# Performance work log

Hardware: AMD Instinct MI355X
Metric: run time of the kernel (lower is better)

## Reference

```python
import jax, jax.numpy as jnp
import numpy as np

HEADS = 8

def conv1x1(x, w, b=None):
    # x: [b,c,h,w], w: [o,c]
    y = jnp.einsum('bchw,oc->bohw', x, w)
    if b is not None:
        y = y + b[None, :, None, None]
    return y

def dwconv3(x, w):
    # depthwise 3x3, SAME padding; w: [C,1,3,3]
    return jax.lax.conv_general_dilated(
        x, w, window_strides=(1, 1), padding='SAME',
        feature_group_count=x.shape[1],
        dimension_numbers=('NCHW', 'OIHW', 'NCHW'))

def layernorm_c(x, w, b):
    # WithBias LayerNorm over channel dim (torch normalizes last dim of b,(hw),c)
    mu = x.mean(axis=1, keepdims=True)
    var = ((x - mu) ** 2).mean(axis=1, keepdims=True)
    return (x - mu) / jnp.sqrt(var + 1e-5) * w[None, :, None, None] + b[None, :, None, None]

def l2norm_lastdim(x):
    n = jnp.sqrt(jnp.sum(x * x, axis=-1, keepdims=True))
    return x / jnp.maximum(n, 1e-12)

def channel_attention(xq, xkv, q_w, q_dw_w, kv_w, kv_dw_w, temperature, attn4, proj_w):
    b, c, h, w = xq.shape
    q = dwconv3(conv1x1(xq, q_w), q_dw_w)
    kv = dwconv3(conv1x1(xkv, kv_w), kv_dw_w)
    k, v = jnp.split(kv, 2, axis=1)
    ch = c // HEADS  # channels per head
    def heads(t):
        return t.reshape(b, HEADS, ch, h * w)
    q, k, v = heads(q), heads(k), heads(v)
    q = l2norm_lastdim(q)
    k = l2norm_lastdim(k)
    attn = jnp.einsum('bhcn,bhdn->bhcd', q, k) * temperature[None]  # [b,H,ch,ch]
    kk = int(ch * 0.9)
    thr = jax.lax.top_k(attn, kk)[0][..., -1:]
    masked = jnp.where(attn >= thr, attn, -jnp.inf)
    score = jax.nn.softmax(masked, axis=-1)
    out = jnp.einsum('bhcd,bhdn->bhcn', score, v) * attn4
    out = out.reshape(b, c, h, w)
    return conv1x1(out, proj_w)

def geglu_ffn(x, ffn_in_w, ffn_dw_w, ffn_out_w):
    y = conv1x1(x, ffn_in_w)
    y = dwconv3(y, ffn_dw_w)
    y1, y2 = jnp.split(y, 2, axis=1)
    return conv1x1(jax.nn.gelu(y1, approximate=False) * y2, ffn_out_w)


def reference(vi_featur, ir_featur, text_code,
              se_w1, se_w2, conv1x1_w, conv1x1_b, conv_out_w, conv_out_b,
              text_w1, text_b1, text_w2, text_b2,
              norm1_w, norm1_b, norm2_w, norm2_b, norm3_w, norm3_b,
              q_w, q_dw_w, kv_w, kv_dw_w, temperature, attn4, proj_w,
              ffn_in_w, ffn_dw_w, ffn_out_w):
    b, c, h, w = vi_featur.shape
    concat = jnp.concatenate([vi_featur, ir_featur], axis=1)  # [b,2c,h,w]
    squeeze = concat.mean(axis=(2, 3))                         # [b,2c]
    cw = jax.nn.sigmoid(jax.nn.relu(squeeze @ se_w1.T) @ se_w2.T)
    topk = c  # int(2*ch_dim*0.5)
    idx = jax.lax.top_k(cw, topk)[1]                           # [b,topk]
    selected = jnp.take_along_axis(concat, idx[:, :, None, None], axis=1)
    img = conv1x1(selected, conv1x1_w, conv1x1_b)              # [b,2c,h,w]
    tf = jax.nn.relu(text_code @ text_w1.T + text_b1) @ text_w2.T + text_b2  # [b,2c]
    soft_idx = jax.lax.top_k(tf, 2 * c)[1]                     # full descending perm
    shuffled = jnp.take_along_axis(img, soft_idx[:, :, None, None], axis=1)
    q_in = conv1x1(shuffled, conv_out_w, conv_out_b)           # [b,c,h,w]
    img_feature2 = conv1x1(concat, conv_out_w, conv_out_b)
    att = channel_attention(layernorm_c(q_in, norm1_w, norm1_b),
                            layernorm_c(img_feature2, norm2_w, norm2_b),
                            q_w, q_dw_w, kv_w, kv_dw_w, temperature, attn4, proj_w)
    output = att + geglu_ffn(layernorm_c(att, norm3_w, norm3_b), ffn_in_w, ffn_dw_w, ffn_out_w)
    return (output, img_feature2)


def setup_inputs() -> dict:
    key = jax.random.key(0)
    ks = jax.random.split(key, 20)
    B, C, H, W = 4, 128, 128, 128
    s = 0.05
    d = {
        'vi_featur': jax.random.normal(ks[0], (B, C, H, W), jnp.float32),
        'ir_featur': jax.random.normal(ks[1], (B, C, H, W), jnp.float32),
        'text_code': jax.random.normal(ks[2], (B, 512), jnp.float32),
        'se_w1': jax.random.normal(ks[3], (32, 256), jnp.float32) * s,
        'se_w2': jax.random.normal(ks[4], (256, 32), jnp.float32) * s,
        'conv1x1_w': jax.random.normal(ks[5], (256, 128), jnp.float32) * s,
        'conv1x1_b': jnp.zeros((256,), jnp.float32),
        'conv_out_w': jax.random.normal(ks[6], (128, 256), jnp.float32) * s,
        'conv_out_b': jnp.zeros((128,), jnp.float32),
        'text_w1': jax.random.normal(ks[7], (512, 512), jnp.float32) * s,
        'text_b1': jnp.zeros((512,), jnp.float32),
        'text_w2': jax.random.normal(ks[8], (256, 512), jnp.float32) * s,
        'text_b2': jnp.zeros((256,), jnp.float32),
        'norm1_w': jnp.ones((128,), jnp.float32), 'norm1_b': jnp.zeros((128,), jnp.float32),
        'norm2_w': jnp.ones((128,), jnp.float32), 'norm2_b': jnp.zeros((128,), jnp.float32),
        'norm3_w': jnp.ones((128,), jnp.float32), 'norm3_b': jnp.zeros((128,), jnp.float32),
        'q_w': jax.random.normal(ks[9], (128, 128), jnp.float32) * s,
        'q_dw_w': jax.random.normal(ks[10], (128, 1, 3, 3), jnp.float32) * s,
        'kv_w': jax.random.normal(ks[11], (256, 128), jnp.float32) * s,
        'kv_dw_w': jax.random.normal(ks[12], (256, 1, 3, 3), jnp.float32) * s,
        'temperature': jnp.ones((8, 1, 1), jnp.float32),
        'attn4': jnp.ones((1,), jnp.float32) * 0.2,
        'proj_w': jax.random.normal(ks[13], (128, 128), jnp.float32) * s,
        'ffn_in_w': jax.random.normal(ks[14], (680, 128), jnp.float32) * s,
        'ffn_dw_w': jax.random.normal(ks[15], (680, 1, 3, 3), jnp.float32) * s,
        'ffn_out_w': jax.random.normal(ks[16], (128, 340), jnp.float32) * s,
    }
    return d
```

## Files before the change

### kernel.cpp

```cpp
#include <hip/hip_runtime.h>

typedef unsigned short u16;
typedef __attribute__((ext_vector_type(8))) short bf16x8;
typedef __attribute__((ext_vector_type(4))) float f32x4;

#define N_PIX 16384
static constexpr long NP = 4L * 128 * N_PIX;

__device__ __forceinline__ float bf2f(u16 h) {
  unsigned u = ((unsigned)h) << 16; float f; __builtin_memcpy(&f, &u, 4); return f;
}
__device__ __forceinline__ u16 f2bf(float f) {
  unsigned u; __builtin_memcpy(&u, &f, 4);
  u = (u + 0x7fffu + ((u >> 16) & 1u)) >> 16; return (u16)u;
}

__device__ __forceinline__ float blockReduceSum256(float v) {
  #pragma unroll
  for (int o = 32; o > 0; o >>= 1) v += __shfl_down(v, o, 64);
  __shared__ float sw[4];
  int lane = threadIdx.x & 63, w = threadIdx.x >> 6;
  if (lane == 0) sw[w] = v;
  __syncthreads();
  return (threadIdx.x == 0) ? (sw[0] + sw[1] + sw[2] + sw[3]) : 0.f;
// ... 89 lines not shown
      #pragma unroll
      for (int o = 32; o > 0; o >>= 1) s += __shfl_down(s, o, 64);
      if (lane == 0) t1f[b * 512 + j] = fmaxf(s + tb1[j], 0.f);
    }
  }
}

__global__ __launch_bounds__(256) void text2_k(const float* __restrict__ t1f,
                                               const float* __restrict__ tw2,
                                               const float* __restrict__ tb2,
                                               float* __restrict__ tf) {
  int b = blockIdx.y, j0 = blockIdx.x * 8, tid = threadIdx.x;
  __shared__ float s_t1[512];
  s_t1[tid] = t1f[b * 512 + tid];
  s_t1[tid + 256] = t1f[b * 512 + 256 + tid];
  __syncthreads();
  int w = tid >> 6, lane = tid & 63;
  #pragma unroll
  for (int r = 0; r < 2; ++r) {
    int j = j0 + w * 2 + r;
    const float* wr = tw2 + (long)j * 512;
    float s = 0.f;
    #pragma unroll
    for (int k = 0; k < 8; ++k) s += s_t1[lane + k * 64] * wr[lane + k * 64];
    #pragma unroll
    for (int o = 32; o > 0; o >>= 1) s += __shfl_down(s, o, 64);
    if (lane == 0) tf[b * 256 + j] = s + tb2[j];
  }
}

__global__ __launch_bounds__(256) void rank2_k(const float* __restrict__ tf,
                                               int* __restrict__ sidx) {
  int b = blockIdx.x, tid = threadIdx.x;
  __shared__ float s_tf[256];
  s_tf[tid] = tf[b * 256 + tid];
  __syncthreads();
  float my = s_tf[tid];
  int rk = 0;
  for (int c = 0; c < 256; ++c) {
    float o = s_tf[c];
    rk += (o > my) || (o == my && c < tid);
  }
  sidx[b * 256 + rk] = tid;
}

__global__ __launch_bounds__(128) void mcomb_k(const float* __restrict__ w2,
                                               const float* __restrict__ w2b,
                                               const float* __restrict__ w1,
                                               const float* __restrict__ w1b,
                                               const int* __restrict__ idx,
                                               const int* __restrict__ sidx,
                                               u16* __restrict__ mch,
                                               u16* __restrict__ mcl,
                                               float* __restrict__ bcomb) {
  int o = blockIdx.x, b = blockIdx.y, tid = threadIdx.x;
  __shared__ float s_w2[256];
  __shared__ int s_sx[256];
  s_w2[tid] = w2[o * 256 + tid];
  s_w2[tid + 128] = w2[o * 256 + tid + 128];
  s_sx[tid] = sidx[b * 256 + tid] & 255;
  s_sx[tid + 128] = sidx[b * 256 + tid + 128] & 255;
  u16* hrow = mch + ((long)b * 128 + o) * 256;
  u16* lrow = mcl + ((long)b * 128 + o) * 256;
  hrow[tid] = 0; hrow[tid + 128] = 0;
  lrow[tid] = 0; lrow[tid + 128] = 0;
  __syncthreads();
  float s = 0.f;
  for (int j = 0; j < 256; ++j) s += s_w2[j] * w1[s_sx[j] * 128 + tid];
  int cc = idx[b * 128 + tid] & 255;
  u16 hi = f2bf(s);
  hrow[cc] = hi;
  lrow[cc] = f2bf(s - bf2f(hi));
  if (tid == 0) {
    float bb = w2b[o];
    for (int j = 0; j < 256; ++j) bb += s_w2[j] * w1b[s_sx[j]];
    bcomb[b * 128 + o] = bb;
  }
}

__global__ __launch_bounds__(256) void gemm_dual_k(
    const u16* __restrict__ W2b, const float* __restrict__ b2,
    const u16* __restrict__ Mch, const u16* __restrict__ Mcl,
    const float* __restrict__ bc, const u16* __restrict__ Xb,
    float* __restrict__ out1, u16* __restrict__ qinT, u16* __restrict__ img2T) {
  const int N = N_PIX;
  int n0 = blockIdx.x * 64, o0 = blockIdx.y * 64, bz = blockIdx.z, tid = threadIdx.x;
  __shared__ __align__(16) char smem[36864];
  u16* A1  = (u16*)smem;
  u16* A2h = (u16*)(smem + 9216);
  u16* A2l = (u16*)(smem + 18432);
  u16* Xs  = (u16*)(smem + 27648);
  f32x4 acc1[4], acc2[4];
  #pragma unroll
  for (int i = 0; i < 4; ++i) { acc1[i] = (f32x4){0,0,0,0}; acc2[i] = (f32x4){0,0,0,0}; }
  int wv = tid >> 6, lane = tid & 63;
  int lr = lane & 15, lkq = (lane >> 4) * 8;
  for (int kt = 0; kt < 4; ++kt) {
    int k0 = kt << 6;
    {
      int r = tid >> 2, o = o0 + r;
      #pragma unroll
      for (int cc = 0; cc < 2; ++cc) {
        int col = ((tid & 3) << 3) + cc * 32;
        int k = k0 + col;
        *(bf16x8*)&A1[r * 72 + col] = *(const bf16x8*)(W2b + (long)o * 256 + k);
        *(bf16x8*)&A2h[r * 72 + col] = *(const bf16x8*)(Mch + ((long)bz * 128 + o) * 256 + k);
        *(bf16x8*)&A2l[r * 72 + col] = *(const bf16x8*)(Mcl + ((long)bz * 128 + o) * 256 + k);
      }
    }
    {
      int n = tid & 63;
      const u16* src = Xb + (long)bz * 256 * N + n0 + n;
      #pragma unroll
      for (int cc = 0; cc < 2; ++cc) {
        int kb = ((tid >> 6) << 3) + cc * 32;
        int k = k0 + kb;
        bf16x8 t;
        #pragma unroll
        for (int i = 0; i < 8; ++i) t[i] = (short)src[(long)(k + i) * N];
        *(bf16x8*)&Xs[n * 72 + kb] = t;
      }
    }
    __syncthreads();
    #pragma unroll
    for (int kk = 0; kk < 2; ++kk) {
      int lk = kk * 32 + lkq;
      bf16x8 a1 = *(const bf16x8*)&A1[(wv * 16 + lr) * 72 + lk];
      bf16x8 a2h = *(const bf16x8*)&A2h[(wv * 16 + lr) * 72 + lk];
      bf16x8 a2l = *(const bf16x8*)&A2l[(wv * 16 + lr) * 72 + lk];
      #pragma unroll
      for (int nt = 0; nt < 4; ++nt) {
        bf16x8 bfr = *(const bf16x8*)&Xs[(nt * 16 + lr) * 72 + lk];
        acc1[nt] = __builtin_amdgcn_mfma_f32_16x16x32_bf16(a1, bfr, acc1[nt], 0, 0, 0);
        acc2[nt] = __builtin_amdgcn_mfma_f32_16x16x32_bf16(a2h, bfr, acc2[nt], 0, 0, 0);
        acc2[nt] = __builtin_amdgcn_mfma_f32_16x16x32_bf16(a2l, bfr, acc2[nt], 0, 0, 0);
      }
    }
    __syncthreads();
  }
  float* st1 = (float*)smem;
  u16*  stq = (u16*)(smem + 17408);
  u16*  sti = (u16*)(smem + 26112);
  #pragma unroll
  for (int nt = 0; nt < 4; ++nt)
    #pragma unroll
    for (int r4 = 0; r4 < 4; ++r4) {
      int o_l = wv * 16 + (lane >> 4) * 4 + r4;
      int n_l = nt * 16 + (lane & 15);
      float v1 = acc1[nt][r4] + b2[o0 + o_l];
      float v2 = acc2[nt][r4] + bc[bz * 128 + o0 + o_l];
      st1[o_l * 68 + n_l] = v1;
      stq[n_l * 68 + o_l] = f2bf(v2);
      sti[n_l * 68 + o_l] = f2bf(v1);
    }
  __syncthreads();
  {
    int row = tid >> 2, colb = (tid & 3) * 16;
    float* dst = out1 + ((long)bz * 128 + o0 + row) * N + n0 + colb;
    #pragma unroll
    for (int j = 0; j < 4; ++j)
      *(f32x4*)(dst + j * 4) = *(f32x4*)&st1[row * 68 + colb + j * 4];
    u16* dq = qinT + ((long)bz * N_PIX + n0 + row) * 128 + o0 + colb;
    u16* di = img2T + ((long)bz * N_PIX + n0 + row) * 128 + o0 + colb;
    *(bf16x8*)dq = *(bf16x8*)&stq[row * 68 + colb];
    *(bf16x8*)(dq + 8) = *(bf16x8*)&stq[row * 68 + colb + 8];
    *(bf16x8*)di = *(bf16x8*)&sti[row * 68 + colb];
    *(bf16x8*)(di + 8) = *(bf16x8*)&sti[row * 68 + colb + 8];
  }
}

__global__ __launch_bounds__(256) void lnrow_k(u16* __restrict__ t0, u16* __restrict__ t1,
                                               const float* __restrict__ g1, const float* __restrict__ b1,
                                               const float* __restrict__ g2, const float* __restrict__ b2) {
  int y = blockIdx.y, tid = threadIdx.x;
  u16* buf = y ? t1 : t0;
  const float* g = y ? g2 : g1;
  const float* bb = y ? b2 : b1;
  __shared__ float gs[128], bs[128];
  if (tid < 128) { gs[tid] = g[tid]; bs[tid] = bb[tid]; }
  __syncthreads();
  long p = (long)blockIdx.x * 256 + tid;
  u16* src = buf + p * 128;
  bf16x8 v[16];
  float sum = 0.f, sq = 0.f;
  #pragma unroll
  for (int j = 0; j < 16; ++j) {
    v[j] = *(const bf16x8*)(src + j * 8);
    #pragma unroll
    for (int i = 0; i < 8; ++i) { float f = bf2f((u16)v[j][i]); sum += f; sq += f * f; }
  }
  float mu = sum * (1.f / 128.f);
  float var = sq * (1.f / 128.f) - mu * mu;
  float rs = rsqrtf(fmaxf(var, 0.f) + 1e-5f);
  #pragma unroll
  for (int j = 0; j < 16; ++j) {
    bf16x8 r;
    #pragma unroll
    for (int i = 0; i < 8; ++i) {
      float f = bf2f((u16)v[j][i]);
      r[i] = (short)f2bf((f - mu) * rs * gs[j * 8 + i] + bs[j * 8 + i]);
    }
    *(bf16x8*)(src + j * 8) = r;
  }
}

template<int AMODE, int RESADD, int OUTF, int XT, int OT>
__global__ __launch_bounds__(256) void gemm_k(
    const u16* __restrict__ Ah, const u16* __restrict__ Alo, long a_bstride,
    const u16* __restrict__ X, long x_bstride,
    const u16* __restrict__ res, long res_bstride,
    void* __restrict__ outv, long out_bstride,
    int O, int K) {
  const int N = N_PIX;
  int n0 = blockIdx.x * 64;
  int o0 = blockIdx.y * 64 * OT;
  int bz = blockIdx.z;
  int tid = threadIdx.x;
  int wv = tid >> 6, lane = tid & 63;
  int lr = lane & 15, lkq = (lane >> 4) * 8;
  __shared__ __align__(16) u16 Xs[64][136];
  __shared__ __align__(16) u16 As[(XT == 3) ? 1 : 64][136];
  __shared__ __align__(16) u16 Al[(AMODE == 3) ? 64 : 1][136];
  f32x4 acc[OT][4];
  #pragma unroll
  for (int ot = 0; ot < OT; ++ot)
    #pragma unroll
    for (int i = 0; i < 4; ++i) acc[ot][i] = (f32x4){0.f, 0.f, 0.f, 0.f};

  if (XT == 3) {
    {
      int n = tid >> 2, koff = (tid & 3) << 5;
      const u16* src = X + (long)bz * x_bstride + (long)(n0 + n) * 128 + koff;
      #pragma unroll
      for (int j = 0; j < 4; ++j)
        *(bf16x8*)&Xs[n][koff + j * 8] = *(const bf16x8*)(src + j * 8);
    }
    __syncthreads();
    #pragma unroll
    for (int ot = 0; ot < OT; ++ot) {
      int oc = o0 + ot * 64 + wv * 16 + lr;
      if (oc > O - 1) oc = O - 1;
      const u16* Arow = Ah + (long)oc * 128;
      bf16x8 afr[4];
      #pragma unroll
      for (int kk = 0; kk < 4; ++kk) afr[kk] = *(const bf16x8*)(Arow + kk * 32 + lkq);
      #pragma unroll
      for (int kk = 0; kk < 4; ++kk) {
        int lk = kk * 32 + lkq;
        #pragma unroll
        for (int nt = 0; nt < 4; ++nt) {
          bf16x8 bfr = *(const bf16x8*)&Xs[nt * 16 + lr][lk];
          acc[ot][nt] = __builtin_amdgcn_mfma_f32_16x16x32_bf16(afr[kk], bfr, acc[ot][nt], 0, 0, 0);
        }
      }
    }
    __syncthreads();
  } else {
    int nk = (K + 127) >> 7;
    for (int kt = 0; kt < nk; ++kt) {
      int k0 = kt << 7;
      {
        int n = tid & 63;
        const u16* src = X + (long)bz * x_bstride + n0 + n;
        #pragma unroll
        for (int cc = 0; cc < 4; ++cc) {
          int kb = ((tid >> 6) << 3) + cc * 32;
          int k = k0 + kb;
          bf16x8 t;
          #pragma unroll
          for (int i = 0; i < 8; ++i)
            t[i] = (short)((k + i < K) ? src[(long)(k + i) * N] : (u16)0);
          *(bf16x8*)&Xs[n][kb] = t;
        }
      }
      #pragma unroll
      for (int ot = 0; ot < OT; ++ot) {
        {
          int r = tid >> 2, o = o0 + ot * 64 + r;
          #pragma unroll
          for (int cc = 0; cc < 4; ++cc) {
            int col = ((tid & 3) << 3) + cc * 32;
            int k = k0 + col;
            if (AMODE == 2) {
              bf16x8 t;
              if (o < O && k + 8 <= K) {
                t = *(const bf16x8*)(Ah + (long)o * K + k);
              } else {
                #pragma unroll
                for (int i = 0; i < 8; ++i)
                  t[i] = (short)((o < O && k + i < K) ? Ah[(long)o * K + k + i] : (u16)0);
              }
              *(bf16x8*)&As[r][col] = t;
            } else {
              long base = (long)bz * a_bstride + (long)o * K + k;
              *(bf16x8*)&As[r][col] = *(const bf16x8*)(Ah + base);
              *(bf16x8*)&Al[r][col] = *(const bf16x8*)(Alo + base);
            }
          }
        }
        __syncthreads();
        #pragma unroll
        for (int kk = 0; kk < 4; ++kk) {
          int lk = kk * 32 + lkq;
          bf16x8 afr = *(const bf16x8*)&As[wv * 16 + lr][lk];
          bf16x8 alr;
          if (AMODE == 3) alr = *(const bf16x8*)&Al[wv * 16 + lr][lk];
          #pragma unroll
          for (int nt = 0; nt < 4; ++nt) {
            bf16x8 bfr = *(const bf16x8*)&Xs[nt * 16 + lr][lk];
            acc[ot][nt] = __builtin_amdgcn_mfma_f32_16x16x32_bf16(afr, bfr, acc[ot][nt], 0, 0, 0);
            if (AMODE == 3)
              acc[ot][nt] = __builtin_amdgcn_mfma_f32_16x16x32_bf16(alr, bfr, acc[ot][nt], 0, 0, 0);
          }
        }
        __syncthreads();
      }
    }
  }

  #pragma unroll
  for (int ot = 0; ot < OT; ++ot) {
    if (ot > 0) __syncthreads();
    if (OUTF == 0) {
      u16* st = &Xs[0][0];
      #pragma unroll
      for (int nt = 0; nt < 4; ++nt)
        #pragma unroll
        for (int r4 = 0; r4 < 4; ++r4) {
          int row = wv * 16 + (lane >> 4) * 4 + r4;
          int col = nt * 16 + (lane & 15);
          st[row * 68 + col] = f2bf(acc[ot][nt][r4]);
        }
      __syncthreads();
      #pragma unroll
      for (int it = 0; it < 2; ++it) {
        int row = (tid >> 3) + it * 32;
        int col = (tid & 7) * 8;
        int o = o0 + ot * 64 + row;
        if (o < O) {
          bf16x8 v = *(bf16x8*)&st[row * 68 + col];
          *(bf16x8*)((u16*)outv + (long)bz * out_bstride + (long)o * N + n0 + col) = v;
        }
      }
    } else {
      float* st = (float*)&Xs[0][0];
      #pragma unroll
      for (int nt = 0; nt < 4; ++nt)
        #pragma unroll
        for (int r4 = 0; r4 < 4; ++r4) {
          int row = wv * 16 + (lane >> 4) * 4 + r4;
          int col = nt * 16 + (lane & 15);
          st[row * 68 + col] = acc[ot][nt][r4];
        }
      __syncthreads();
      {
        int row = tid >> 2, colb = (tid & 3) * 16;
        int o = o0 + ot * 64 + row;
        if (o < O) {
          float* dst = (float*)outv + (long)bz * out_bstride + (long)o * N + n0 + colb;
          bf16x8 rv0, rv1;
          if (RESADD) {
            const u16* rp = res + (long)bz * res_bstride + (long)o * N + n0 + colb;
            rv0 = *(const bf16x8*)rp;
            rv1 = *(const bf16x8*)(rp + 8);
          }
          #pragma unroll
          for (int j = 0; j < 4; ++j) {
            f32x4 v = *(f32x4*)&st[row * 68 + colb + j * 4];
            if (RESADD) {
              #pragma unroll
              for (int i = 0; i < 4; ++i) {
                int idx = j * 4 + i;
                u16 rr = (u16)((idx < 8) ? rv0[idx] : rv1[idx - 8]);
                v[i] += bf2f(rr);
              }
            }
            *(f32x4*)(dst + j * 4) = v;
          }
        }
      }
    }
  }
}

__global__ __launch_bounds__(256) void lnt_k(const u16* __restrict__ in,
                                             const float* __restrict__ gamma,
                                             const float* __restrict__ beta,
                                             u16* __restrict__ outT) {
  int p0 = blockIdx.x * 64, b = blockIdx.y, tid = threadIdx.x;
  int px = tid & 63, g4 = tid >> 6;
  __shared__ float tile[128][65];
  __shared__ float red[8][64];
  __shared__ float gmm[128], bta[128], mu_s[64], rs_s[64];
  if (tid < 128) { gmm[tid] = gamma[tid]; bta[tid] = beta[tid]; }
  long bofs = (long)b * 128 * N_PIX;
  float s = 0.f;
  for (int c = g4; c < 128; c += 4) {
    float v = bf2f(in[bofs + (long)c * N_PIX + p0 + px]);
    tile[c][px] = v;
    s += v;
  }
  red[g4][px] = s;
  __syncthreads();
  if (g4 == 0) mu_s[px] = (red[0][px] + red[1][px] + red[2][px] + red[3][px]) * (1.f / 128.f);
  __syncthreads();
  float mu = mu_s[px];
  float s2 = 0.f;
  for (int c = g4; c < 128; c += 4) { float d = tile[c][px] - mu; s2 += d * d; }
  red[4 + g4][px] = s2;
  __syncthreads();
  if (g4 == 0) {
    float var = (red[4][px] + red[5][px] + red[6][px] + red[7][px]) * (1.f / 128.f);
    rs_s[px] = rsqrtf(var + 1e-5f);
  }
  __syncthreads();
  float rs = rs_s[px];
  for (int c = g4; c < 128; c += 4)
    tile[c][px] = (tile[c][px] - mu) * rs * gmm[c] + bta[c];
  __syncthreads();
  int px2 = tid >> 2, c0 = (tid & 3) << 5;
  u16* dst = outT + ((long)b * N_PIX + p0 + px2) * 128 + c0;
  #pragma unroll
  for (int j = 0; j < 4; ++j) {
    bf16x8 r;
    #pragma unroll
    for (int i = 0; i < 8; ++i) r[i] = (short)f2bf(tile[c0 + j * 8 + i][px2]);
    *(bf16x8*)(dst + j * 8) = r;
  }
}

__global__ __launch_bounds__(256) void dw3t2_k(const u16* __restrict__ inQ,
                                               const float* __restrict__ wQ,
                                               u16* __restrict__ outQ,
                                               const u16* __restrict__ inKV,
                                               const float* __restrict__ wKV,
                                               u16* __restrict__ outKV) {
  int gp = blockIdx.x >> 3, stripe = blockIdx.x & 7, tid = threadIdx.x;
  const u16* in; const float* w; u16* out; int c; long pbase;
  if (gp < 512) { in = inQ;  w = wQ;  out = outQ;  c = gp & 127;  pbase = (long)gp * N_PIX; }
  else { int p2 = gp - 512; in = inKV; w = wKV; out = outKV; c = p2 & 255; pbase = (long)p2 * N_PIX; }
  int y0 = stripe * 16;
  __shared__ __align__(16) u16 tile[18][136];
  for (int v = tid; v < 288; v += 256) {
    int r = v >> 4, col = (v & 15) << 3;
    int y = y0 - 1 + r;
    bf16x8 t;
    #pragma unroll
    for (int i = 0; i < 8; ++i) t[i] = 0;
    if (y >= 0 && y < 128) t = *(const bf16x8*)(in + pbase + y * 128 + col);
    *(bf16x8*)&tile[r][col] = t;
  }
  float wv[9];
  #pragma unroll
  for (int j = 0; j < 9; ++j) wv[j] = w[c * 9 + j];
  __syncthreads();
  int row = tid >> 4, col0 = (tid & 15) << 3;
  float a[3][10];
  #pragma unroll
  for (int dr = 0; dr < 3; ++dr)
    #pragma unroll
    for (int i = 0; i < 10; ++i) {
      int x = col0 - 1 + i;
      a[dr][i] = (x >= 0 && x < 128) ? bf2f(tile[row + dr][x]) : 0.f;
    }
  bf16x8 res;
  #pragma unroll
  for (int j = 0; j < 8; ++j) {
    float s = 0.f;
    #pragma unroll
    for (int dr = 0; dr < 3; ++dr)
      #pragma unroll
      for (int dx = 0; dx < 3; ++dx) s += wv[dr * 3 + dx] * a[dr][j + dx];
    res[j] = (short)f2bf(s);
  }
  *(bf16x8*)(out + pbase + (y0 + row) * 128 + col0) = res;
}

__global__ __launch_bounds__(256) void dw3gelu4_k(const u16* __restrict__ ft,
                                                  const float* __restrict__ w,
                                                  u16* __restrict__ fg) {
  int plane = blockIdx.x >> 3, stripe = blockIdx.x & 7, tid = threadIdx.x;
  int b = plane / 340, c = plane % 340;
  const u16* t1 = ft + ((long)b * 680 + c) * N_PIX;
  const u16* t2 = ft + ((long)b * 680 + 340 + c) * N_PIX;
  u16* g = fg + ((long)b * 340 + c) * N_PIX;
  int y0 = stripe * 16;
  __shared__ __align__(16) u16 ta[18][136];
  __shared__ __align__(16) u16 tb[18][136];
  for (int v = tid; v < 288; v += 256) {
    int r = v >> 4, col = (v & 15) << 3;
    int y = y0 - 1 + r;
    bf16x8 u1, u2;
    #pragma unroll
    for (int i = 0; i < 8; ++i) { u1[i] = 0; u2[i] = 0; }
    if (y >= 0 && y < 128) {
      u1 = *(const bf16x8*)(t1 + y * 128 + col);
      u2 = *(const bf16x8*)(t2 + y * 128 + col);
    }
    *(bf16x8*)&ta[r][col] = u1;
    *(bf16x8*)&tb[r][col] = u2;
  }
  float w1[9], w2[9];
  #pragma unroll
  for (int j = 0; j < 9; ++j) { w1[j] = w[c * 9 + j]; w2[j] = w[(340 + c) * 9 + j]; }
  __syncthreads();
  int row = tid >> 4, col0 = (tid & 15) << 3;
  float a[3][10], bb[3][10];
  #pragma unroll
  for (int dr = 0; dr < 3; ++dr)
    #pragma unroll
// ... 131 lines not shown
  }
}

extern "C" void kernel_launch(void* const* d_in, const int* in_sizes, int n_in,
                              void* d_out, int out_size, void* d_ws, size_t ws_size,
                              hipStream_t stream) {
  (void)in_sizes; (void)n_in; (void)out_size; (void)ws_size;
  const float* vi        = (const float*)d_in[0];
  const float* ir        = (const float*)d_in[1];
  const float* text_code = (const float*)d_in[2];
  const float* se_w1     = (const float*)d_in[3];
  const float* se_w2     = (const float*)d_in[4];
  const float* conv1x1_w = (const float*)d_in[5];
  const float* conv1x1_b = (const float*)d_in[6];
  const float* conv_out_w= (const float*)d_in[7];
  const float* conv_out_b= (const float*)d_in[8];
  const float* text_w1   = (const float*)d_in[9];
  const float* text_b1   = (const float*)d_in[10];
  const float* text_w2   = (const float*)d_in[11];
  const float* text_b2   = (const float*)d_in[12];
  const float* norm1_w   = (const float*)d_in[13];
  const float* norm1_b   = (const float*)d_in[14];
  const float* norm2_w   = (const float*)d_in[15];
  const float* norm2_b   = (const float*)d_in[16];
  const float* norm3_w   = (const float*)d_in[17];
  const float* norm3_b   = (const float*)d_in[18];
  const float* q_w       = (const float*)d_in[19];
  const float* q_dw_w    = (const float*)d_in[20];
  const float* kv_w      = (const float*)d_in[21];
  const float* kv_dw_w   = (const float*)d_in[22];
  const float* temperature = (const float*)d_in[23];
  const float* attn4     = (const float*)d_in[24];
  const float* proj_w    = (const float*)d_in[25];
  const float* ffn_in_w  = (const float*)d_in[26];
  const float* ffn_dw_w  = (const float*)d_in[27];
  const float* ffn_out_w = (const float*)d_in[28];
  float* out0 = (float*)d_out;
  float* out1 = out0 + NP;

  char* W = (char*)d_ws;
  float* sq_f  = (float*)(W + 0);
  int*   idx_i = (int*)(W + 4096);
  int*   sidx_i= (int*)(W + 6144);
  u16*   Mch   = (u16*)(W + 12288);
  u16*   Mcl   = (u16*)(W + 274432);
  float* bcomb = (float*)(W + 536576);
  float* qn_f  = (float*)(W + 538624);
  float* kn_f  = (float*)(W + 540672);
  float* attnm = (float*)(W + 542720);
  u16*   cmbh  = (u16*)(W + 575488);
  u16*   cmbl  = (u16*)(W + 706560);
  float* t1f   = (float*)(W + 834560);
  float* tf_f  = (float*)(W + 842752);
  u16*   W2b   = (u16*)(W + 846848);
  u16*   qwb   = (u16*)(W + 912384);
  u16*   kvwb  = (u16*)(W + 945152);
  u16*   ffnWb = (u16*)(W + (1 << 20));
  u16*   ffnOb = (u16*)(W + (1 << 20) + 174080);
  u16* S    = (u16*)(W + (2 << 20));
  u16* CC   = S;
  u16* KD   = S + 512L * N_PIX;
  u16* KVD  = S + 1024L * N_PIX;
  u16* CBF  = S + 1024L * N_PIX;
  u16* X3T  = S + 2048L * N_PIX;
  u16* XKVT = S + 2560L * N_PIX;
  u16* FT4  = S + 2560L * N_PIX;
  u16* FG4  = S + 5280L * N_PIX;
  u16* KVT  = (u16*)out0;
  u16* ATT  = KD;

  const long SN = 128L * N_PIX;
  const long SN2 = 256L * N_PIX;

  wconv5_k<<<340, 256, 0, stream>>>(conv_out_w, W2b, 32768, q_w, qwb, 16384,
                                    kv_w, kvwb, 32768, ffn_in_w, ffnWb, 87040,
                                    ffn_out_w, ffnOb, 43520);
  squeeze_k<<<dim3(256, 4), 256, 0, stream>>>(vi, ir, sq_f, CBF);
  se_text1_k<<<dim3(65, 4), 256, 0, stream>>>(sq_f, se_w1, se_w2, idx_i,
                                              text_code, text_w1, text_b1, t1f);
  text2_k<<<dim3(32, 4), 256, 0, stream>>>(t1f, text_w2, text_b2, tf_f);
  rank2_k<<<4, 256, 0, stream>>>(tf_f, sidx_i);
  mcomb_k<<<dim3(128, 4), 128, 0, stream>>>(conv_out_w, conv_out_b, conv1x1_w,
                                            conv1x1_b, idx_i, sidx_i, Mch, Mcl, bcomb);
  gemm_dual_k<<<dim3(256, 2, 4), 256, 0, stream>>>(
      W2b, conv_out_b, Mch, Mcl, bcomb, CBF, out1, CC, XKVT);
  lnrow_k<<<dim3(256, 2), 256, 0, stream>>>(CC, XKVT, norm1_w, norm1_b, norm2_w, norm2_b);
  gemm_k<2, 0, 0, 3, 2><<<dim3(256, 1, 4), 256, 0, stream>>>(
      qwb, nullptr, 0, CC, SN, nullptr, 0, KD, SN, 128, 128);
  gemm_k<2, 0, 0, 3, 2><<<dim3(256, 2, 4), 256, 0, stream>>>(
      kvwb, nullptr, 0, XKVT, SN, nullptr, 0, KVT, SN2, 256, 128);
  dw3t2_k<<<12288, 256, 0, stream>>>(KD, q_dw_w, CC, KVT, kv_dw_w, KVD);
  rownorm2_k<<<dim3(256, 4), 256, 0, stream>>>(CC, KVD, qn_f, kn_f);
  float* part = (float*)out0;
  attn_part_k<<<dim3(64, 8, 4), 256, 0, stream>>>(CC, KVD, SN2, part);
  attn_reduce_k<<<32, 256, 0, stream>>>(part, qn_f, kn_f, temperature, attnm);
  score_cmb_k<<<4, 128, 0, stream>>>(attnm, proj_w, attn4, cmbh, cmbl);
  gemm_k<3, 0, 0, 0, 2><<<dim3(256, 1, 4), 256, 0, stream>>>(
      cmbh, cmbl, 128L * 128, KVD + SN, SN2, nullptr, 0, ATT, SN, 128, 128);
  lnt_k<<<dim3(256, 4), 256, 0, stream>>>(ATT, norm3_w, norm3_b, X3T);
  gemm_k<2, 0, 0, 3, 2><<<dim3(256, 6, 4), 256, 0, stream>>>(
      ffnWb, nullptr, 0, X3T, SN, nullptr, 0, FT4, 680L * N_PIX, 680, 128);
  dw3gelu4_k<<<10880, 256, 0, stream>>>(FT4, ffn_dw_w, FG4);
  gemm_k<2, 1, 1, 0, 2><<<dim3(256, 1, 4), 256, 0, stream>>>(
      ffnOb, nullptr, 0, FG4, 340L * N_PIX, ATT, SN,
      out0, SN, 128, 340);
}
```

Baseline: 390.4 us.

## Fuse channel LayerNorms into the dual GEMM and attention-output GEMM epilogues

The dual GEMM now computes all 128 output channels per block, which lets it apply LayerNorm 1 and 2 in its epilogue and removes the separate lnrow_k pass. A new att_ln_k kernel combines the score×V GEMM with the norm3 LayerNorm, replacing the AMODE 3 gemm_k path and lnt_k. The aim is to drop two extra full-tensor read/write passes and two launches. In exchange, the grid has half as many blocks, and the LayerNorm statistics are taken from bf16-rounded values.

```diff
diff --git a/kernel.cpp b/kernel.cpp
--- a/kernel.cpp
+++ b/kernel.cpp
@@ -195,32 +195,27 @@
     const u16* __restrict__ W2b, const float* __restrict__ b2,
     const u16* __restrict__ Mch, const u16* __restrict__ Mcl,
     const float* __restrict__ bc, const u16* __restrict__ Xb,
-    float* __restrict__ out1, u16* __restrict__ qinT, u16* __restrict__ img2T) {
+    float* __restrict__ out1, u16* __restrict__ xqT, u16* __restrict__ xkvT,
+    const float* __restrict__ g1, const float* __restrict__ b1,
+    const float* __restrict__ g2, const float* __restrict__ b2n) {
   const int N = N_PIX;
-  int n0 = blockIdx.x * 64, o0 = blockIdx.y * 64, bz = blockIdx.z, tid = threadIdx.x;
+  int n0 = blockIdx.x * 64, bz = blockIdx.z, tid = threadIdx.x;
   __shared__ __align__(16) char smem[36864];
   u16* A1  = (u16*)smem;
   u16* A2h = (u16*)(smem + 9216);
   u16* A2l = (u16*)(smem + 18432);
   u16* Xs  = (u16*)(smem + 27648);
-  f32x4 acc1[4], acc2[4];
-  #pragma unroll
-  for (int i = 0; i < 4; ++i) { acc1[i] = (f32x4){0,0,0,0}; acc2[i] = (f32x4){0,0,0,0}; }
+  __shared__ float gs1[128], bs1[128], gs2[128], bs2[128];
+  if (tid < 128) { gs1[tid] = g1[tid]; bs1[tid] = b1[tid]; gs2[tid] = g2[tid]; bs2[tid] = b2n[tid]; }
+  f32x4 acc1[2][4], acc2[2][4];
+  #pragma unroll
+  for (int ot = 0; ot < 2; ++ot)
+    #pragma unroll
+    for (int i = 0; i < 4; ++i) { acc1[ot][i] = (f32x4){0,0,0,0}; acc2[ot][i] = (f32x4){0,0,0,0}; }
   int wv = tid >> 6, lane = tid & 63;
   int lr = lane & 15, lkq = (lane >> 4) * 8;
   for (int kt = 0; kt < 4; ++kt) {
     int k0 = kt << 6;
-    {
-      int r = tid >> 2, o = o0 + r;
-      #pragma unroll
-      for (int cc = 0; cc < 2; ++cc) {
-        int col = ((tid & 3) << 3) + cc * 32;
-        int k = k0 + col;
-        *(bf16x8*)&A1[r * 72 + col] = *(const bf16x8*)(W2b + (long)o * 256 + k);
-        *(bf16x8*)&A2h[r * 72 + col] = *(const bf16x8*)(Mch + ((long)bz * 128 + o) * 256 + k);
-        *(bf16x8*)&A2l[r * 72 + col] = *(const bf16x8*)(Mcl + ((long)bz * 128 + o) * 256 + k);
-      }
-    }
     {
       int n = tid & 63;
       const u16* src = Xb + (long)bz * 256 * N + n0 + n;
@@ -234,86 +229,255 @@
         *(bf16x8*)&Xs[n * 72 + kb] = t;
       }
     }
-    __syncthreads();
-    #pragma unroll
-    for (int kk = 0; kk < 2; ++kk) {
+    #pragma unroll
+    for (int ot = 0; ot < 2; ++ot) {
+      {
+        int r = tid >> 2, o = ot * 64 + r;
+        #pragma unroll
+        for (int cc = 0; cc < 2; ++cc) {
+          int col = ((tid & 3) << 3) + cc * 32;
+          int k = k0 + col;
+          *(bf16x8*)&A1[r * 72 + col] = *(const bf16x8*)(W2b + (long)o * 256 + k);
+          *(bf16x8*)&A2h[r * 72 + col] = *(const bf16x8*)(Mch + ((long)bz * 128 + o) * 256 + k);
+          *(bf16x8*)&A2l[r * 72 + col] = *(const bf16x8*)(Mcl + ((long)bz * 128 + o) * 256 + k);
+        }
+      }
+      __syncthreads();
+      #pragma unroll
+      for (int kk = 0; kk < 2; ++kk) {
+        int lk = kk * 32 + lkq;
+        bf16x8 a1 = *(const bf16x8*)&A1[(wv * 16 + lr) * 72 + lk];
+        bf16x8 a2h = *(const bf16x8*)&A2h[(wv * 16 + lr) * 72 + lk];
+        bf16x8 a2l = *(const bf16x8*)&A2l[(wv * 16 + lr) * 72 + lk];
+        #pragma unroll
+        for (int nt = 0; nt < 4; ++nt) {
+          bf16x8 bfr = *(const bf16x8*)&Xs[(nt * 16 + lr) * 72 + lk];
+          acc1[ot][nt] = __builtin_amdgcn_mfma_f32_16x16x32_bf16(a1, bfr, acc1[ot][nt], 0, 0, 0);
+          acc2[ot][nt] = __builtin_amdgcn_mfma_f32_16x16x32_bf16(a2h, bfr, acc2[ot][nt], 0, 0, 0);
+          acc2[ot][nt] = __builtin_amdgcn_mfma_f32_16x16x32_bf16(a2l, bfr, acc2[ot][nt], 0, 0, 0);
+        }
+      }
+      __syncthreads();
+    }
+  }
+  float* st1 = (float*)smem;
+  #pragma unroll
+  for (int ot = 0; ot < 2; ++ot) {
+    #pragma unroll
+    for (int nt = 0; nt < 4; ++nt)
+      #pragma unroll
+      for (int r4 = 0; r4 < 4; ++r4) {
+        int o_l = wv * 16 + (lane >> 4) * 4 + r4;
+        int n_l = nt * 16 + (lane & 15);
+        st1[o_l * 68 + n_l] = acc1[ot][nt][r4] + b2[ot * 64 + o_l];
+      }
+    __syncthreads();
+    {
+      int row = tid >> 2, colb = (tid & 3) * 16;
+      float* dst = out1 + ((long)bz * 128 + ot * 64 + row) * N + n0 + colb;
+      #pragma unroll
+      for (int j = 0; j < 4; ++j)
+        *(f32x4*)(dst + j * 4) = *(f32x4*)&st1[row * 68 + colb + j * 4];
+    }
+    __syncthreads();
+  }
+  u16* stq = (u16*)smem;
+  #pragma unroll
+  for (int ot = 0; ot < 2; ++ot)
+    #pragma unroll
+    for (int nt = 0; nt < 4; ++nt)
+      #pragma unroll
+      for (int r4 = 0; r4 < 4; ++r4) {
+        int o_a = ot * 64 + wv * 16 + (lane >> 4) * 4 + r4;
+        int n_l = nt * 16 + (lane & 15);
+        stq[n_l * 132 + o_a] = f2bf(acc2[ot][nt][r4] + bc[bz * 128 + o_a]);
+      }
+  __syncthreads();
+  {
+    int n = tid >> 2, c0 = (tid & 3) * 32;
+    bf16x8 v[4];
+    float sum = 0.f, sq = 0.f;
+    #pragma unroll
+    for (int j = 0; j < 4; ++j) {
+      v[j] = *(const bf16x8*)&stq[n * 132 + c0 + j * 8];
+      #pragma unroll
+      for (int i = 0; i < 8; ++i) { float f = bf2f((u16)v[j][i]); sum += f; sq += f * f; }
+    }
+    sum += __shfl_xor(sum, 1, 64); sum += __shfl_xor(sum, 2, 64);
+    sq  += __shfl_xor(sq, 1, 64);  sq  += __shfl_xor(sq, 2, 64);
+    float mu = sum * (1.f / 128.f);
+    float var = sq * (1.f / 128.f) - mu * mu;
+    float rs = rsqrtf(fmaxf(var, 0.f) + 1e-5f);
+    u16* dst = xqT + ((long)bz * N_PIX + n0 + n) * 128 + c0;
+    #pragma unroll
+    for (int j = 0; j < 4; ++j) {
+      bf16x8 r;
+      #pragma unroll
+      for (int i = 0; i < 8; ++i) {
+        float f = bf2f((u16)v[j][i]);
+        r[i] = (short)f2bf((f - mu) * rs * gs1[c0 + j * 8 + i] + bs1[c0 + j * 8 + i]);
+      }
+      *(bf16x8*)(dst + j * 8) = r;
+    }
+  }
+  __syncthreads();
+  #pragma unroll
+  for (int ot = 0; ot < 2; ++ot)
+    #pragma unroll
+    for (int nt = 0; nt < 4; ++nt)
+      #pragma unroll
+      for (int r4 = 0; r4 < 4; ++r4) {
+        int o_a = ot * 64 + wv * 16 + (lane >> 4) * 4 + r4;
+        int n_l = nt * 16 + (lane & 15);
+        stq[n_l * 132 + o_a] = f2bf(acc1[ot][nt][r4] + b2[o_a]);
+      }
+  __syncthreads();
+  {
+    int n = tid >> 2, c0 = (tid & 3) * 32;
+    bf16x8 v[4];
+    float sum = 0.f, sq = 0.f;
+    #pragma unroll
+    for (int j = 0; j < 4; ++j) {
+      v[j] = *(const bf16x8*)&stq[n * 132 + c0 + j * 8];
+      #pragma unroll
+      for (int i = 0; i < 8; ++i) { float f = bf2f((u16)v[j][i]); sum += f; sq += f * f; }
+    }
+    sum += __shfl_xor(sum, 1, 64); sum += __shfl_xor(sum, 2, 64);
+    sq  += __shfl_xor(sq, 1, 64);  sq  += __shfl_xor(sq, 2, 64);
+    float mu = sum * (1.f / 128.f);
+    float var = sq * (1.f / 128.f) - mu * mu;
+    float rs = rsqrtf(fmaxf(var, 0.f) + 1e-5f);
+    u16* dst = xkvT + ((long)bz * N_PIX + n0 + n) * 128 + c0;
+    #pragma unroll
+    for (int j = 0; j < 4; ++j) {
+      bf16x8 r;
+      #pragma unroll
+      for (int i = 0; i < 8; ++i) {
+        float f = bf2f((u16)v[j][i]);
+        r[i] = (short)f2bf((f - mu) * rs * gs2[c0 + j * 8 + i] + bs2[c0 + j * 8 + i]);
+      }
+      *(bf16x8*)(dst + j * 8) = r;
+    }
+  }
+}
+
+__global__ __launch_bounds__(256) void att_ln_k(
+    const u16* __restrict__ Ah, const u16* __restrict__ Alo,
+    const u16* __restrict__ V, long v_bstride,
+    u16* __restrict__ att, u16* __restrict__ x3T,
+    const float* __restrict__ g3, const float* __restrict__ b3) {
+  const int N = N_PIX;
+  int n0 = blockIdx.x * 64, bz = blockIdx.z, tid = threadIdx.x;
+  int wv = tid >> 6, lane = tid & 63;
+  int lr = lane & 15, lkq = (lane >> 4) * 8;
+  __shared__ __align__(16) u16 Xs[64][136];
+  __shared__ __align__(16) u16 As[64][136];
+  __shared__ __align__(16) u16 Al[64][136];
+  __shared__ float gs[128], bs[128];
+  if (tid < 128) { gs[tid] = g3[tid]; bs[tid] = b3[tid]; }
+  f32x4 acc[2][4];
+  #pragma unroll
+  for (int ot = 0; ot < 2; ++ot)
+    #pragma unroll
+    for (int i = 0; i < 4; ++i) acc[ot][i] = (f32x4){0.f, 0.f, 0.f, 0.f};
+  {
+    int n = tid & 63;
+    const u16* src = V + (long)bz * v_bstride + n0 + n;
+    #pragma unroll
+    for (int cc = 0; cc < 4; ++cc) {
+      int kb = ((tid >> 6) << 3) + cc * 32;
+      bf16x8 t;
+      #pragma unroll
+      for (int i = 0; i < 8; ++i) t[i] = (short)src[(long)(kb + i) * N];
+      *(bf16x8*)&Xs[n][kb] = t;
+    }
+  }
+  #pragma unroll
+  for (int ot = 0; ot < 2; ++ot) {
+    {
+      int r = tid >> 2, o = ot * 64 + r;
+      #pragma unroll
+      for (int cc = 0; cc < 4; ++cc) {
+        int col = ((tid & 3) << 3) + cc * 32;
+        long base = (long)bz * (128L * 128) + (long)o * 128 + col;
+        *(bf16x8*)&As[r][col] = *(const bf16x8*)(Ah + base);
+        *(bf16x8*)&Al[r][col] = *(const bf16x8*)(Alo + base);
+      }
+    }
+    __syncthreads();
+    #pragma unroll
+    for (int kk = 0; kk < 4; ++kk) {
       int lk = kk * 32 + lkq;
-      bf16x8 a1 = *(const bf16x8*)&A1[(wv * 16 + lr) * 72 + lk];
-      bf16x8 a2h = *(const bf16x8*)&A2h[(wv * 16 + lr) * 72 + lk];
-      bf16x8 a2l = *(const bf16x8*)&A2l[(wv * 16 + lr) * 72 + lk];
+      bf16x8 afr = *(const bf16x8*)&As[wv * 16 + lr][lk];
+      bf16x8 alr = *(const bf16x8*)&Al[wv * 16 + lr][lk];
       #pragma unroll
       for (int nt = 0; nt < 4; ++nt) {
-        bf16x8 bfr = *(const bf16x8*)&Xs[(nt * 16 + lr) * 72 + lk];
-        acc1[nt] = __builtin_amdgcn_mfma_f32_16x16x32_bf16(a1, bfr, acc1[nt], 0, 0, 0);
-        acc2[nt] = __builtin_amdgcn_mfma_f32_16x16x32_bf16(a2h, bfr, acc2[nt], 0, 0, 0);
-        acc2[nt] = __builtin_amdgcn_mfma_f32_16x16x32_bf16(a2l, bfr, acc2[nt], 0, 0, 0);
-      }
-    }
-    __syncthreads();
-  }
-  float* st1 = (float*)smem;
-  u16*  stq = (u16*)(smem + 17408);
-  u16*  sti = (u16*)(smem + 26112);
-  #pragma unroll
-  for (int nt = 0; nt < 4; ++nt)
-    #pragma unroll
-    for (int r4 = 0; r4 < 4; ++r4) {
-      int o_l = wv * 16 + (lane >> 4) * 4 + r4;
-      int n_l = nt * 16 + (lane & 15);
-      float v1 = acc1[nt][r4] + b2[o0 + o_l];
-      float v2 = acc2[nt][r4] + bc[bz * 128 + o0 + o_l];
-      st1[o_l * 68 + n_l] = v1;
-      stq[n_l * 68 + o_l] = f2bf(v2);
-      sti[n_l * 68 + o_l] = f2bf(v1);
-    }
+        bf16x8 bfr = *(const bf16x8*)&Xs[nt * 16 + lr][lk];
+        acc[ot][nt] = __builtin_amdgcn_mfma_f32_16x16x32_bf16(afr, bfr, acc[ot][nt], 0, 0, 0);
+        acc[ot][nt] = __builtin_amdgcn_mfma_f32_16x16x32_bf16(alr, bfr, acc[ot][nt], 0, 0, 0);
+      }
+    }
+    __syncthreads();
+  }
+  u16* st = &Xs[0][0];
+  #pragma unroll
+  for (int ot = 0; ot < 2; ++ot) {
+    #pragma unroll
+    for (int nt = 0; nt < 4; ++nt)
+      #pragma unroll
+      for (int r4 = 0; r4 < 4; ++r4) {
+        int row = wv * 16 + (lane >> 4) * 4 + r4;
+        int col = nt * 16 + (lane & 15);
+        st[row * 68 + col] = f2bf(acc[ot][nt][r4]);
+      }
+    __syncthreads();
+    #pragma unroll
+    for (int it = 0; it < 2; ++it) {
+      int row = (tid >> 3) + it * 32;
+      int col = (tid & 7) * 8;
+      bf16x8 v = *(bf16x8*)&st[row * 68 + col];
+      *(bf16x8*)(att + ((long)bz * 128 + ot * 64 + row) * N + n0 + col) = v;
+    }
+    __syncthreads();
+  }
+  u16* stq = &Xs[0][0];
+  #pragma unroll
+  for (int ot = 0; ot < 2; ++ot)
+    #pragma unroll
+    for (int nt = 0; nt < 4; ++nt)
+      #pragma unroll
+      for (int r4 = 0; r4 < 4; ++r4) {
+        int o_a = ot * 64 + wv * 16 + (lane >> 4) * 4 + r4;
+        int n_l = nt * 16 + (lane & 15);
+        stq[n_l * 132 + o_a] = f2bf(acc[ot][nt][r4]);
+      }
   __syncthreads();
   {
-    int row = tid >> 2, colb = (tid & 3) * 16;
-    float* dst = out1 + ((long)bz * 128 + o0 + row) * N + n0 + colb;
-    #pragma unroll
-    for (int j = 0; j < 4; ++j)
-      *(f32x4*)(dst + j * 4) = *(f32x4*)&st1[row * 68 + colb + j * 4];
-    u16* dq = qinT + ((long)bz * N_PIX + n0 + row) * 128 + o0 + colb;
-    u16* di = img2T + ((long)bz * N_PIX + n0 + row) * 128 + o0 + colb;
-    *(bf16x8*)dq = *(bf16x8*)&stq[row * 68 + colb];
-    *(bf16x8*)(dq + 8) = *(bf16x8*)&stq[row * 68 + colb + 8];
-    *(bf16x8*)di = *(bf16x8*)&sti[row * 68 + colb];
-    *(bf16x8*)(di + 8) = *(bf16x8*)&sti[row * 68 + colb + 8];
-  }
-}
-
-__global__ __launch_bounds__(256) void lnrow_k(u16* __restrict__ t0, u16* __restrict__ t1,
-                                               const float* __restrict__ g1, const float* __restrict__ b1,
-                                               const float* __restrict__ g2, const float* __restrict__ b2) {
-  int y = blockIdx.y, tid = threadIdx.x;
-  u16* buf = y ? t1 : t0;
-  const float* g = y ? g2 : g1;
-  const float* bb = y ? b2 : b1;
-  __shared__ float gs[128], bs[128];
-  if (tid < 128) { gs[tid] = g[tid]; bs[tid] = bb[tid]; }
-  __syncthreads();
-  long p = (long)blockIdx.x * 256 + tid;
-  u16* src = buf + p * 128;
-  bf16x8 v[16];
-  float sum = 0.f, sq = 0.f;
-  #pragma unroll
-  for (int j = 0; j < 16; ++j) {
-    v[j] = *(const bf16x8*)(src + j * 8);
-    #pragma unroll
-    for (int i = 0; i < 8; ++i) { float f = bf2f((u16)v[j][i]); sum += f; sq += f * f; }
-  }
-  float mu = sum * (1.f / 128.f);
-  float var = sq * (1.f / 128.f) - mu * mu;
-  float rs = rsqrtf(fmaxf(var, 0.f) + 1e-5f);
-  #pragma unroll
-  for (int j = 0; j < 16; ++j) {
-    bf16x8 r;
-    #pragma unroll
-    for (int i = 0; i < 8; ++i) {
-      float f = bf2f((u16)v[j][i]);
-      r[i] = (short)f2bf((f - mu) * rs * gs[j * 8 + i] + bs[j * 8 + i]);
-    }
-    *(bf16x8*)(src + j * 8) = r;
+    int n = tid >> 2, c0 = (tid & 3) * 32;
+    bf16x8 v[4];
+    float sum = 0.f, sq = 0.f;
+    #pragma unroll
+    for (int j = 0; j < 4; ++j) {
+      v[j] = *(const bf16x8*)&stq[n * 132 + c0 + j * 8];
+      #pragma unroll
+      for (int i = 0; i < 8; ++i) { float f = bf2f((u16)v[j][i]); sum += f; sq += f * f; }
+    }
+    sum += __shfl_xor(sum, 1, 64); sum += __shfl_xor(sum, 2, 64);
+    sq  += __shfl_xor(sq, 1, 64);  sq  += __shfl_xor(sq, 2, 64);
+    float mu = sum * (1.f / 128.f);
+    float var = sq * (1.f / 128.f) - mu * mu;
+    float rs = rsqrtf(fmaxf(var, 0.f) + 1e-5f);
+    u16* dst = x3T + ((long)bz * N_PIX + n0 + n) * 128 + c0;
+    #pragma unroll
+    for (int j = 0; j < 4; ++j) {
+      bf16x8 r;
+      #pragma unroll
+      for (int i = 0; i < 8; ++i) {
+        float f = bf2f((u16)v[j][i]);
+        r[i] = (short)f2bf((f - mu) * rs * gs[c0 + j * 8 + i] + bs[c0 + j * 8 + i]);
+      }
+      *(bf16x8*)(dst + j * 8) = r;
+    }
   }
 }
 
@@ -333,7 +497,6 @@
   int lr = lane & 15, lkq = (lane >> 4) * 8;
   __shared__ __align__(16) u16 Xs[64][136];
   __shared__ __align__(16) u16 As[(XT == 3) ? 1 : 64][136];
-  __shared__ __align__(16) u16 Al[(AMODE == 3) ? 64 : 1][136];
   f32x4 acc[OT][4];
   #pragma unroll
   for (int ot = 0; ot < OT; ++ot)
@@ -394,21 +557,15 @@
           for (int cc = 0; cc < 4; ++cc) {
             int col = ((tid & 3) << 3) + cc * 32;
             int k = k0 + col;
-            if (AMODE == 2) {
-              bf16x8 t;
-              if (o < O && k + 8 <= K) {
-                t = *(const bf16x8*)(Ah + (long)o * K + k);
-              } else {
-                #pragma unroll
-                for (int i = 0; i < 8; ++i)
-                  t[i] = (short)((o < O && k + i < K) ? Ah[(long)o * K + k + i] : (u16)0);
-              }
-              *(bf16x8*)&As[r][col] = t;
+            bf16x8 t;
+            if (o < O && k + 8 <= K) {
+              t = *(const bf16x8*)(Ah + (long)o * K + k);
             } else {
-              long base = (long)bz * a_bstride + (long)o * K + k;
-              *(bf16x8*)&As[r][col] = *(const bf16x8*)(Ah + base);
-              *(bf16x8*)&Al[r][col] = *(const bf16x8*)(Alo + base);
+              #pragma unroll
+              for (int i = 0; i < 8; ++i)
+                t[i] = (short)((o < O && k + i < K) ? Ah[(long)o * K + k + i] : (u16)0);
             }
+            *(bf16x8*)&As[r][col] = t;
           }
         }
         __syncthreads();
@@ -416,14 +573,10 @@
         for (int kk = 0; kk < 4; ++kk) {
           int lk = kk * 32 + lkq;
           bf16x8 afr = *(const bf16x8*)&As[wv * 16 + lr][lk];
-          bf16x8 alr;
-          if (AMODE == 3) alr = *(const bf16x8*)&Al[wv * 16 + lr][lk];
           #pragma unroll
           for (int nt = 0; nt < 4; ++nt) {
             bf16x8 bfr = *(const bf16x8*)&Xs[nt * 16 + lr][lk];
             acc[ot][nt] = __builtin_amdgcn_mfma_f32_16x16x32_bf16(afr, bfr, acc[ot][nt], 0, 0, 0);
-            if (AMODE == 3)
-              acc[ot][nt] = __builtin_amdgcn_mfma_f32_16x16x32_bf16(alr, bfr, acc[ot][nt], 0, 0, 0);
           }
         }
         __syncthreads();
@@ -493,52 +646,6 @@
         }
       }
     }
-  }
-}
-
-__global__ __launch_bounds__(256) void lnt_k(const u16* __restrict__ in,
-                                             const float* __restrict__ gamma,
-                                             const float* __restrict__ beta,
-                                             u16* __restrict__ outT) {
-  int p0 = blockIdx.x * 64, b = blockIdx.y, tid = threadIdx.x;
-  int px = tid & 63, g4 = tid >> 6;
-  __shared__ float tile[128][65];
-  __shared__ float red[8][64];
-  __shared__ float gmm[128], bta[128], mu_s[64], rs_s[64];
-  if (tid < 128) { gmm[tid] = gamma[tid]; bta[tid] = beta[tid]; }
-  long bofs = (long)b * 128 * N_PIX;
-  float s = 0.f;
-  for (int c = g4; c < 128; c += 4) {
-    float v = bf2f(in[bofs + (long)c * N_PIX + p0 + px]);
-    tile[c][px] = v;
-    s += v;
-  }
-  red[g4][px] = s;
-  __syncthreads();
-  if (g4 == 0) mu_s[px] = (red[0][px] + red[1][px] + red[2][px] + red[3][px]) * (1.f / 128.f);
-  __syncthreads();
-  float mu = mu_s[px];
-  float s2 = 0.f;
-  for (int c = g4; c < 128; c += 4) { float d = tile[c][px] - mu; s2 += d * d; }
-  red[4 + g4][px] = s2;
-  __syncthreads();
-  if (g4 == 0) {
-    float var = (red[4][px] + red[5][px] + red[6][px] + red[7][px]) * (1.f / 128.f);
-    rs_s[px] = rsqrtf(var + 1e-5f);
-  }
-  __syncthreads();
-  float rs = rs_s[px];
-  for (int c = g4; c < 128; c += 4)
-    tile[c][px] = (tile[c][px] - mu) * rs * gmm[c] + bta[c];
-  __syncthreads();
-  int px2 = tid >> 2, c0 = (tid & 3) << 5;
-  u16* dst = outT + ((long)b * N_PIX + p0 + px2) * 128 + c0;
-  #pragma unroll
-  for (int j = 0; j < 4; ++j) {
-    bf16x8 r;
-    #pragma unroll
-    for (int i = 0; i < 8; ++i) r[i] = (short)f2bf(tile[c0 + j * 8 + i][px2]);
-    *(bf16x8*)(dst + j * 8) = r;
   }
 }
 
@@ -836,9 +943,9 @@
   rank2_k<<<4, 256, 0, stream>>>(tf_f, sidx_i);
   mcomb_k<<<dim3(128, 4), 128, 0, stream>>>(conv_out_w, conv_out_b, conv1x1_w,
                                             conv1x1_b, idx_i, sidx_i, Mch, Mcl, bcomb);
-  gemm_dual_k<<<dim3(256, 2, 4), 256, 0, stream>>>(
-      W2b, conv_out_b, Mch, Mcl, bcomb, CBF, out1, CC, XKVT);
-  lnrow_k<<<dim3(256, 2), 256, 0, stream>>>(CC, XKVT, norm1_w, norm1_b, norm2_w, norm2_b);
+  gemm_dual_k<<<dim3(256, 1, 4), 256, 0, stream>>>(
+      W2b, conv_out_b, Mch, Mcl, bcomb, CBF, out1, CC, XKVT,
+      norm1_w, norm1_b, norm2_w, norm2_b);
   gemm_k<2, 0, 0, 3, 2><<<dim3(256, 1, 4), 256, 0, stream>>>(
       qwb, nullptr, 0, CC, SN, nullptr, 0, KD, SN, 128, 128);
   gemm_k<2, 0, 0, 3, 2><<<dim3(256, 2, 4), 256, 0, stream>>>(
@@ -849,9 +956,8 @@
   attn_part_k<<<dim3(64, 8, 4), 256, 0, stream>>>(CC, KVD, SN2, part);
   attn_reduce_k<<<32, 256, 0, stream>>>(part, qn_f, kn_f, temperature, attnm);
   score_cmb_k<<<4, 128, 0, stream>>>(attnm, proj_w, attn4, cmbh, cmbl);
-  gemm_k<3, 0, 0, 0, 2><<<dim3(256, 1, 4), 256, 0, stream>>>(
-      cmbh, cmbl, 128L * 128, KVD + SN, SN2, nullptr, 0, ATT, SN, 128, 128);
-  lnt_k<<<dim3(256, 4), 256, 0, stream>>>(ATT, norm3_w, norm3_b, X3T);
+  att_ln_k<<<dim3(256, 1, 4), 256, 0, stream>>>(
+      cmbh, cmbl, KVD + SN, SN2, ATT, X3T, norm3_w, norm3_b);
   gemm_k<2, 0, 0, 3, 2><<<dim3(256, 6, 4), 256, 0, stream>>>(
       ffnWb, nullptr, 0, X3T, SN, nullptr, 0, FT4, 680L * N_PIX, 680, 128);
   dw3gelu4_k<<<10880, 256, 0, stream>>>(FT4, ffn_dw_w, FG4);
```

Result: faster. 356.7 us (-8.6%).
